# Performance work log

Measured on AMD Instinct MI355X. Metric: run time of the kernel, lower is better.

The kernel has to match this reference:

```python
import jax, jax.numpy as jnp
import numpy as np

B, S, H = 2, 1024, 4096
NH, DH, NKV = 32, 128, 2          # heads, head_dim, kv groups
ROT = DH // 2                      # 64: GLM rotates first half of head dim
GROUP = NH // NKV                  # 16 query heads per kv group
SCALE = DH ** -0.5


def glm_rope(x, pos):
    """GLM interleaved rotary on first ROT dims. x: [B,S,h,DH], pos: [B,S] int."""
    rot, rest = x[..., :ROT], x[..., ROT:]
    inv_freq = 1.0 / (10000.0 ** (jnp.arange(0, ROT, 2, dtype=jnp.float32) / ROT))  # [ROT/2]
    ang = pos.astype(jnp.float32)[:, :, None] * inv_freq[None, None, :]             # [B,S,ROT/2]
    cos = jnp.cos(ang)[:, :, None, :]
    sin = jnp.sin(ang)[:, :, None, :]
    x0, x1 = rot[..., 0::2], rot[..., 1::2]
    o0 = x0 * cos - x1 * sin
    o1 = x1 * cos + x0 * sin
    rot_out = jnp.stack([o0, o1], axis=-1).reshape(rot.shape)
    return jnp.concatenate([rot_out, rest], axis=-1)


def setup_inputs() -> dict:
    key = jax.random.key(0)
    k1, k2, k3, k4 = jax.random.split(key, 4)
    return {
        "hidden_states": jax.random.normal(k1, (B, S, H), jnp.float32) * 0.02,
        "position_ids": jnp.arange(B * S, dtype=jnp.int32).reshape(B, S) % S,
        "W_qkv": jax.random.normal(k2, (H, NH * DH + 2 * NKV * DH), jnp.float32) * 0.02,
        "b_qkv": jax.random.normal(k3, (NH * DH + 2 * NKV * DH,), jnp.float32) * 0.02,
        "W_dense": jax.random.normal(k4, (NH * DH, H), jnp.float32) * 0.02,
    }


def reference(hidden_states, position_ids, W_qkv, b_qkv, W_dense):
    qkv = hidden_states @ W_qkv + b_qkv                              # [B,S,4608]
    q = qkv[..., : NH * DH].reshape(B, S, NH, DH)
    k = qkv[..., NH * DH : NH * DH + NKV * DH].reshape(B, S, NKV, DH)
    v = qkv[..., NH * DH + NKV * DH :].reshape(B, S, NKV, DH)

    q = glm_rope(q, position_ids)
    k = glm_rope(k, position_ids)

    # GQA: expand kv groups to all heads
    k = jnp.repeat(k, GROUP, axis=2)                                 # [B,S,NH,DH]
    v = jnp.repeat(v, GROUP, axis=2)

    scores = jnp.einsum("bqhd,bkhd->bhqk", q, k) * SCALE             # [B,NH,S,S]
    causal = jnp.tril(jnp.ones((S, S), dtype=bool))
    scores = jnp.where(causal[None, None], scores, jnp.finfo(scores.dtype).min)
    probs = jax.nn.softmax(scores, axis=-1)
    ctx = jnp.einsum("bhqk,bkhd->bqhd", probs, v).reshape(B, S, NH * DH)
    return ctx @ W_dense                                             # [B,S,H]
```

## Files before the change

kernel.cpp:

```cpp
#include <hip/hip_runtime.h>

#define B_    2
#define S_    1024
#define H_    4096
#define NH_   32
#define DH_   128
#define NKV_  2
#define GROUP_ 16
#define ROT_  64
#define NQKV_ 4608
#define SCALE_ 0.08838834764831845f
#define KVB   64

typedef __attribute__((ext_vector_type(8))) short bf16x8;
typedef __attribute__((ext_vector_type(4))) float f32x4;

typedef __attribute__((address_space(1))) const void* gptr_t;
typedef __attribute__((address_space(3))) void* lptr_t;

__device__ __forceinline__ unsigned short f2bf(float f) {
    unsigned int u = __builtin_bit_cast(unsigned int, f);
    u += 0x7FFFu + ((u >> 16) & 1u);
    return (unsigned short)(u >> 16);
}
__device__ __forceinline__ unsigned int pack2bf(float a, float b) {
    return (unsigned int)f2bf(a) | ((unsigned int)f2bf(b) << 16);
}

__global__ void k_f32_to_bf16(const float* __restrict__ in,
                              unsigned short* __restrict__ out, int n4) {
    int i = blockIdx.x * blockDim.x + threadIdx.x;
    if (i >= n4) return;
    const float4 v = reinterpret_cast<const float4*>(in)[i];
    ushort4 o;
    o.x = f2bf(v.x); o.y = f2bf(v.y); o.z = f2bf(v.z); o.w = f2bf(v.w);
    reinterpret_cast<ushort4*>(out)[i] = o;
}

__global__ __launch_bounds__(256) void k_transpose_bf16(
    const float* __restrict__ in, unsigned short* __restrict__ out,
    int K, int N) {
    __shared__ float tile[64][69];
    const int n0 = blockIdx.x * 64, k0 = blockIdx.y * 64;
    const int t = threadIdx.x;
    const int lk = t >> 4, ln4 = (t & 15) * 4;
    #pragma unroll
    for (int i = 0; i < 4; i++) {
        const float4 v = *reinterpret_cast<const float4*>(
            in + (size_t)(k0 + lk + i * 16) * N + n0 + ln4);
        tile[lk + i * 16][ln4 + 0] = v.x;
        tile[lk + i * 16][ln4 + 1] = v.y;
        tile[lk + i * 16][ln4 + 2] = v.z;
        tile[lk + i * 16][ln4 + 3] = v.w;
    }
    __syncthreads();
    const int n = t >> 2, kc = (t & 3) * 16;
    unsigned short tmp[16];
    #pragma unroll
    for (int j = 0; j < 16; j++) tmp[j] = f2bf(tile[kc + j][n]);
    unsigned short* dst = out + (size_t)(n0 + n) * K + k0 + kc;
    *reinterpret_cast<uint4*>(dst)     = *reinterpret_cast<uint4*>(tmp);
    *reinterpret_cast<uint4*>(dst + 8) = *reinterpret_cast<uint4*>(tmp + 8);
}

__global__ void k_rope_tab(const int* __restrict__ pos_ids,
                           float2* __restrict__ tab) {
    const int idx = blockIdx.x * blockDim.x + threadIdx.x;
    if (idx >= B_ * S_ * 32) return;
    const int t = idx >> 5, pr = idx & 31;
    const float freq = exp2f(-0.41524101186092f * (float)pr);
    float sn, cs;
    sincosf((float)pos_ids[t] * freq, &sn, &cs);
    tab[idx] = make_float2(cs, sn);
}

template<int MODE>
__global__ __launch_bounds__(256, 2) void k_gemm(
    const unsigned short* __restrict__ A,
    const unsigned short* __restrict__ Bt,
    const float* __restrict__ bias,
    float* __restrict__ Cf,
    const float2* __restrict__ ctab,
    unsigned short* __restrict__ Qh,
    unsigned short* __restrict__ Kh,
    unsigned short* __restrict__ Vt,
    int M, int N, int K)
{
    __shared__ __align__(16) char lds[2][32768];

    const int tid  = threadIdx.x;
    const int wave = tid >> 6, lane = tid & 63;
    const int lrow = lane & 15, lhi = lane >> 4;
    const int wm = (wave >> 1) * 64, wn = (wave & 1) * 64;
    const size_t a_row0 = (size_t)blockIdx.y * 128;
    const size_t b_col0 = (size_t)blockIdx.x * 128;

    const size_t strideK = (size_t)K * 2;
    const char* Asrc = (const char*)A + (a_row0 + (tid >> 3)) * strideK;
    const char* Bsrc = (const char*)Bt + (b_col0 + (tid >> 3)) * strideK;
    const int swz_src = ((tid & 7) * 16) ^ (((tid >> 3) & 7) << 4);
    const int dst_off = tid * 16;

    f32x4 acc[4][4] = {};
    const int nt = K >> 6;

    #pragma unroll
    for (int j = 0; j < 4; j++) {
        __builtin_amdgcn_global_load_lds(
            (gptr_t)(Asrc + (size_t)j * 32 * strideK + swz_src),
            (lptr_t)(lds[0] + j * 4096 + dst_off), 16, 0, 0);
        __builtin_amdgcn_global_load_lds(
            (gptr_t)(Bsrc + (size_t)j * 32 * strideK + swz_src),
            (lptr_t)(lds[0] + 16384 + j * 4096 + dst_off), 16, 0, 0);
    }

    int cur = 0;
    for (int t = 0; t < nt; t++) {
        if (t + 1 < nt) {
            const size_t kb = (size_t)(t + 1) * 128;
            #pragma unroll
            for (int j = 0; j < 4; j++) {
                __builtin_amdgcn_global_load_lds(
                    (gptr_t)(Asrc + (size_t)j * 32 * strideK + kb + swz_src),
                    (lptr_t)(lds[cur ^ 1] + j * 4096 + dst_off), 16, 0, 0);
                __builtin_amdgcn_global_load_lds(
                    (gptr_t)(Bsrc + (size_t)j * 32 * strideK + kb + swz_src),
                    (lptr_t)(lds[cur ^ 1] + 16384 + j * 4096 + dst_off), 16, 0, 0);
            }
            asm volatile("s_waitcnt vmcnt(8)" ::: "memory");
        } else {
            asm volatile("s_waitcnt vmcnt(0)" ::: "memory");
        }
        __builtin_amdgcn_s_barrier();

        const char* La = lds[cur];
        const char* Lb = lds[cur] + 16384;
        bf16x8 af[4][2], bfr[4][2];
        #pragma unroll
        for (int i = 0; i < 4; i++) {
            const int fr = wm + i * 16 + lrow;
            af[i][0] = *(const bf16x8*)(La + fr * 128 + ((lhi * 16) ^ ((fr & 7) << 4)));
            af[i][1] = *(const bf16x8*)(La + fr * 128 + ((64 + lhi * 16) ^ ((fr & 7) << 4)));
        }
        #pragma unroll
        for (int j = 0; j < 4; j++) {
            const int br = wn + j * 16 + lrow;
            bfr[j][0] = *(const bf16x8*)(Lb + br * 128 + ((lhi * 16) ^ ((br & 7) << 4)));
            bfr[j][1] = *(const bf16x8*)(Lb + br * 128 + ((64 + lhi * 16) ^ ((br & 7) << 4)));
        }
        #pragma unroll
        for (int i = 0; i < 4; i++)
            #pragma unroll
            for (int j = 0; j < 4; j++) {
                acc[i][j] = __builtin_amdgcn_mfma_f32_16x16x32_bf16(
                    af[i][0], bfr[j][0], acc[i][j], 0, 0, 0);
                acc[i][j] = __builtin_amdgcn_mfma_f32_16x16x32_bf16(
                    af[i][1], bfr[j][1], acc[i][j], 0, 0, 0);
            }
        __builtin_amdgcn_s_barrier();
        cur ^= 1;
    }

    if (MODE == 0) {
        #pragma unroll
        for (int i = 0; i < 4; i++)
            #pragma unroll
            for (int j = 0; j < 4; j++) {
                const size_t grow0 = a_row0 + wm + i * 16 + lhi * 4;
                const size_t gcol  = b_col0 + wn + j * 16 + lrow;
                const float bi = bias ? bias[gcol] : 0.f;
                #pragma unroll
                for (int r = 0; r < 4; r++)
                    Cf[(grow0 + r) * N + gcol] = acc[i][j][r] + bi;
            }
    } else {
        const int bx = (int)blockIdx.x;
        const size_t bb = a_row0 >> 10;
        if (bx >= 34) {
            const int g = bx - 34;
            #pragma unroll
            for (int i = 0; i < 4; i++)
                #pragma unroll
                for (int j = 0; j < 4; j++) {
                    const int dloc = wn + j * 16 + lrow;
                    const float bi = bias[b_col0 + dloc];
                    const size_t row0 = a_row0 + wm + i * 16 + lhi * 4;
                    unsigned short* dst =
                        Vt + ((bb * NKV_ + g) * DH_ + dloc) * S_ + (row0 & 1023);
                    *reinterpret_cast<uint2*>(dst) = make_uint2(
                        pack2bf(acc[i][j][0] + bi, acc[i][j][1] + bi),
                        pack2bf(acc[i][j][2] + bi, acc[i][j][3] + bi));
                }
        } else {
            unsigned short* lds_c = (unsigned short*)&lds[0][0];
            #pragma unroll
            for (int i = 0; i < 4; i++)
                #pragma unroll
                for (int j = 0; j < 4; j++) {
                    const int dloc = wn + j * 16 + lrow;
                    const float bi = bias[b_col0 + dloc];
                    const int rloc0 = wm + i * 16 + lhi * 4;
                    float v[4];
                    #pragma unroll
                    for (int r = 0; r < 4; r++) v[r] = acc[i][j][r] + bi;
                    if (dloc < 64) {
                        const int pr = dloc >> 1;
                        #pragma unroll
                        for (int r = 0; r < 4; r++) {
                            const float2 cs = ctab[(a_row0 + rloc0 + r) * 32 + pr];
                            const float partner = __shfl_xor(v[r], 1);
                            v[r] = (dloc & 1) ? (v[r] * cs.x + partner * cs.y)
                                              : (v[r] * cs.x - partner * cs.y);
                        }
                    }
                    #pragma unroll
                    for (int r = 0; r < 4; r++)
                        lds_c[(rloc0 + r) * 128 + dloc] = f2bf(v[r]);
                }
            __syncthreads();
            unsigned short* base = (bx < 32)
                ? Qh + ((bb * NH_ + bx) * S_ + (a_row0 & 1023)) * DH_
                : Kh + ((bb * NKV_ + (bx - 32)) * S_ + (a_row0 & 1023)) * DH_;
            const int off = tid * 64;
            #pragma unroll
            for (int c = 0; c < 8; c++)
                *reinterpret_cast<uint4*>(base + off + c * 8) =
                    *reinterpret_cast<const uint4*>(lds_c + off + c * 8);
        }
    }
}

__global__ __launch_bounds__(256) void k_attn(
    const unsigned short* __restrict__ Qh,
    const unsigned short* __restrict__ Kh,
    const unsigned short* __restrict__ Vt,
    unsigned short* __restrict__ ctx)
{
    __shared__ __align__(16) char lds_kt[2][16384];
    __shared__ __align__(16) char lds_vt[16384];
    __shared__ __align__(16) char lds_p[4][2048];

    const int tid  = threadIdx.x;
    const int wave = tid >> 6, lane = tid & 63;
    const int lrow = lane & 15, lhi = lane >> 4;
    char* myp = lds_p[wave];

    const int blk  = blockIdx.x;
    const int pair = blk & 7;
    const int h    = (blk >> 3) & 31;
    const int b    = blk >> 8;
    const int g    = h >> 4;

    const char* Kbase = (const char*)(Kh + (size_t)((b * NKV_ + g) * S_) * DH_);
    const char* Vbase = (const char*)(Vt + (size_t)((b * NKV_ + g) * DH_) * S_);

    const int kcol = lrow * 16;
    const int vrow_l = lane >> 3;
    const int vcol = (lane & 7) * 16;

    for (int half = 0; half < 2; half++) {
        const int qt = half ? (15 - pair) : pair;
        const int q0 = qt * 64 + wave * 16;
        const int ntiles = qt + 1;
        const int q_glob = q0 + lrow;

        #pragma unroll
        for (int i = 0; i < 4; i++) {
            const int ci = wave * 4 + i;
            const int r  = ci * 4 + lhi;
            __builtin_amdgcn_global_load_lds(
                (gptr_t)(Kbase + (size_t)r * 256 + (kcol ^ ((r & 7) << 4))),
                (lptr_t)(lds_kt[0] + ci * 1024), 16, 0, 0);
        }
        const unsigned short* Qp = Qh + ((size_t)((b * NH_ + h) * S_) + q0) * DH_;
        bf16x8 a_q[4];
        #pragma unroll
        for (int ks = 0; ks < 4; ks++)
            a_q[ks] = *(const bf16x8*)(Qp + (size_t)lrow * DH_ + ks * 32 + lhi * 8);
        asm volatile("s_waitcnt vmcnt(0)" ::: "memory");
        __builtin_amdgcn_s_barrier();

        float m_run = -1e30f, l_run = 0.f;
        f32x4 o_acc[8] = {};
        int cur = 0;

        for (int t = 0; t < ntiles; t++) {
            const bool has_next = (t + 1 < ntiles);
            #pragma unroll
            for (int i = 0; i < 4; i++) {
                const int ci = wave * 4 + i;
                const int r  = ci * 8 + vrow_l;
                __builtin_amdgcn_global_load_lds(
                    (gptr_t)(Vbase + (size_t)r * (S_ * 2) + t * (KVB * 2)
                             + (vcol ^ ((r & 7) << 4))),
                    (lptr_t)(lds_vt + ci * 1024), 16, 0, 0);
            }
            if (has_next) {
                const char* ksrc = Kbase + (size_t)(t + 1) * 16384;
                #pragma unroll
                for (int i = 0; i < 4; i++) {
                    const int ci = wave * 4 + i;
                    const int r  = ci * 4 + lhi;
                    __builtin_amdgcn_global_load_lds(
                        (gptr_t)(ksrc + (size_t)r * 256 + (kcol ^ ((r & 7) << 4))),
                        (lptr_t)(lds_kt[cur ^ 1] + ci * 1024), 16, 0, 0);
                }
            }
            f32x4 s_acc[4] = {};
            #pragma unroll
            for (int sub = 0; sub < 4; sub++) {
                const int r = sub * 16 + lrow;
                #pragma unroll
                for (int ks = 0; ks < 4; ks++) {
                    const bf16x8 a_k = *(const bf16x8*)(
                        lds_kt[cur] + r * 256 + ((ks * 64 + lhi * 16) ^ ((r & 7) << 4)));
                    s_acc[sub] = __builtin_amdgcn_mfma_f32_16x16x32_bf16(
                        a_k, a_q[ks], s_acc[sub], 0, 0, 0);
                }
            }
            float pv[16];
            float mx = -1e30f;
            if (!has_next) {
                #pragma unroll
                for (int sub = 0; sub < 4; sub++)
                    #pragma unroll
                    for (int r = 0; r < 4; r++) {
                        const int kvg = t * KVB + sub * 16 + lhi * 4 + r;
                        float sv = s_acc[sub][r] * SCALE_;
                        if (kvg > q_glob) sv = -1e30f;
                        pv[sub * 4 + r] = sv;
                        mx = fmaxf(mx, sv);
                    }
            } else {
                #pragma unroll
                for (int sub = 0; sub < 4; sub++)
                    #pragma unroll
                    for (int r = 0; r < 4; r++) {
                        const float sv = s_acc[sub][r] * SCALE_;
                        pv[sub * 4 + r] = sv;
                        mx = fmaxf(mx, sv);
                    }
            }
            mx = fmaxf(mx, __shfl_xor(mx, 16));
            mx = fmaxf(mx, __shfl_xor(mx, 32));
            const float mnew = fmaxf(m_run, mx);
            const float scale = __expf(m_run - mnew);
            m_run = mnew;
            float sm = 0.f;
            #pragma unroll
            for (int i = 0; i < 16; i++) {
                const float e = __expf(pv[i] - mnew);
                pv[i] = e;
                sm += e;
            }
            sm += __shfl_xor(sm, 16);
            sm += __shfl_xor(sm, 32);
            l_run = l_run * scale + sm;
            #pragma unroll
            for (int d = 0; d < 8; d++) {
                o_acc[d][0] *= scale; o_acc[d][1] *= scale;
                o_acc[d][2] *= scale; o_acc[d][3] *= scale;
            }
            #pragma unroll
            for (int sub = 0; sub < 4; sub++) {
                const int off = (lrow * 128 + sub * 32 + lhi * 8) ^ ((lrow & 7) << 4);
                *reinterpret_cast<uint2*>(myp + off) = make_uint2(
                    pack2bf(pv[sub * 4 + 0], pv[sub * 4 + 1]),
                    pack2bf(pv[sub * 4 + 2], pv[sub * 4 + 3]));
            }
            bf16x8 a_p[2];
            #pragma unroll
            for (int frag = 0; frag < 2; frag++) {
                const int off = (lrow * 128 + frag * 64 + lhi * 16) ^ ((lrow & 7) << 4);
                a_p[frag] = *reinterpret_cast<const bf16x8*>(myp + off);
            }
            if (has_next) asm volatile("s_waitcnt vmcnt(4)" ::: "memory");
            else          asm volatile("s_waitcnt vmcnt(0)" ::: "memory");
            __builtin_amdgcn_s_barrier();
            #pragma unroll
            for (int d = 0; d < 8; d++) {
                const int r = d * 16 + lrow;
                #pragma unroll
                for (int frag = 0; frag < 2; frag++) {
                    const bf16x8 a_v = *(const bf16x8*)(
                        lds_vt + r * 128 + ((frag * 64 + lhi * 16) ^ ((r & 7) << 4)));
                    o_acc[d] = __builtin_amdgcn_mfma_f32_16x16x32_bf16(
                        a_v, a_p[frag], o_acc[d], 0, 0, 0);
                }
            }
            asm volatile("s_waitcnt vmcnt(0)" ::: "memory");
            __builtin_amdgcn_s_barrier();
            cur ^= 1;
        }
        const float inv = 1.f / l_run;
        const size_t row = (size_t)b * S_ + q0 + lrow;
        #pragma unroll
        for (int d = 0; d < 8; d++) {
            unsigned short* dst = ctx + row * (NH_ * DH_) + h * DH_ + d * 16 + lhi * 4;
            *reinterpret_cast<uint2*>(dst) = make_uint2(
                pack2bf(o_acc[d][0] * inv, o_acc[d][1] * inv),
                pack2bf(o_acc[d][2] * inv, o_acc[d][3] * inv));
        }
    }
}

extern "C" void kernel_launch(void* const* d_in, const int* in_sizes, int n_in,
                              void* d_out, int out_size, void* d_ws, size_t ws_size,
                              hipStream_t stream)
{
    const float* hidden  = (const float*)d_in[0];
    const int*   pos_ids = (const int*)d_in[1];
    const float* W_qkv   = (const float*)d_in[2];
    const float* b_qkv   = (const float*)d_in[3];
    const float* W_dense = (const float*)d_in[4];
    float* out = (float*)d_out;

    char* ws = (char*)d_ws;
    unsigned short* Xbf = (unsigned short*)(ws);
    unsigned short* Wqt = (unsigned short*)(ws + 16777216);
    unsigned short* Wdt = (unsigned short*)(ws + 54525952);
    float2*         ctab= (float2*)        (ws + 88080384);
    unsigned short* Qh  = (unsigned short*)(ws + 125829120);
    unsigned short* Kh  = (unsigned short*)(ws + 142606336);
    unsigned short* Vt  = (unsigned short*)(ws + 143654912);
    unsigned short* Ctx = (unsigned short*)(ws + 144703488);

    const int M = B_ * S_;

    k_f32_to_bf16<<<(M * H_ / 4 + 255) / 256, 256, 0, stream>>>(hidden, Xbf, M * H_ / 4);
    k_rope_tab<<<(M * 32 + 255) / 256, 256, 0, stream>>>(pos_ids, ctab);
    k_transpose_bf16<<<dim3(NQKV_ / 64, H_ / 64), 256, 0, stream>>>(W_qkv, Wqt, H_, NQKV_);
    k_transpose_bf16<<<dim3(H_ / 64, H_ / 64), 256, 0, stream>>>(W_dense, Wdt, H_, H_);
    k_gemm<1><<<dim3(NQKV_ / 128, M / 128), 256, 0, stream>>>(
        Xbf, Wqt, b_qkv, nullptr, ctab, Qh, Kh, Vt, M, NQKV_, H_);
    k_attn<<<B_ * NH_ * 8, 256, 0, stream>>>(Qh, Kh, Vt, Ctx);
    k_gemm<0><<<dim3(H_ / 128, M / 128), 256, 0, stream>>>(
        Ctx, Wdt, nullptr, out, nullptr, nullptr, nullptr, nullptr, M, H_, H_);
}
```

Baseline: 269.8 us.

## Use four-stage K=32 LDS ring with one barrier per step in GEMM

Rebuilds the GEMM mainloop from a double-buffered K=64 tile with two barriers per iteration into a 4-slot ring of K=32 tiles, prefetched three stages ahead with graded vmcnt waits and a single barrier per step. The LDS layout packs two rows per 128-byte line with a new XOR swizzle. The aim is deeper latency hiding of global loads and fewer barriers. In exchange it doubles the number of iterations and adds a sync before the epilogue reuses LDS.

```diff
diff --git a/kernel.cpp b/kernel.cpp
--- a/kernel.cpp
+++ b/kernel.cpp
@@ -86,7 +86,7 @@
     unsigned short* __restrict__ Vt,
     int M, int N, int K)
 {
-    __shared__ __align__(16) char lds[2][32768];
+    __shared__ __align__(16) char lds[4 * 16384];
 
     const int tid  = threadIdx.x;
     const int wave = tid >> 6, lane = tid & 63;
@@ -96,70 +96,66 @@
     const size_t b_col0 = (size_t)blockIdx.x * 128;
 
     const size_t strideK = (size_t)K * 2;
-    const char* Asrc = (const char*)A + (a_row0 + (tid >> 3)) * strideK;
-    const char* Bsrc = (const char*)Bt + (b_col0 + (tid >> 3)) * strideK;
-    const int swz_src = ((tid & 7) * 16) ^ (((tid >> 3) & 7) << 4);
-    const int dst_off = tid * 16;
+    const char* Abase = (const char*)A + a_row0 * strideK;
+    const char* Bbase = (const char*)Bt + b_col0 * strideK;
+
+    const int q0 = tid, q1 = tid + 256;
+    const int v0_ = q0 >> 3, cl0 = ((q0 & 7) * 16) ^ ((v0_ & 7) << 4);
+    const int v1_ = q1 >> 3, cl1 = ((q1 & 7) * 16) ^ ((v1_ & 7) << 4);
+    const size_t aoff0 = (size_t)(v0_ * 2 + (cl0 >> 6)) * strideK + (cl0 & 63);
+    const size_t aoff1 = (size_t)(v1_ * 2 + (cl1 >> 6)) * strideK + (cl1 & 63);
 
     f32x4 acc[4][4] = {};
-    const int nt = K >> 6;
-
-    #pragma unroll
-    for (int j = 0; j < 4; j++) {
-        __builtin_amdgcn_global_load_lds(
-            (gptr_t)(Asrc + (size_t)j * 32 * strideK + swz_src),
-            (lptr_t)(lds[0] + j * 4096 + dst_off), 16, 0, 0);
-        __builtin_amdgcn_global_load_lds(
-            (gptr_t)(Bsrc + (size_t)j * 32 * strideK + swz_src),
-            (lptr_t)(lds[0] + 16384 + j * 4096 + dst_off), 16, 0, 0);
+    const int nt = K >> 5;
+
+#define STAGE_(tt) { \
+    const size_t kk = (size_t)(tt) * 64; \
+    char* sl = lds + ((tt) & 3) * 16384; \
+    __builtin_amdgcn_global_load_lds((gptr_t)(Abase + aoff0 + kk), \
+        (lptr_t)(sl + tid * 16), 16, 0, 0); \
+    __builtin_amdgcn_global_load_lds((gptr_t)(Abase + aoff1 + kk), \
+        (lptr_t)(sl + 4096 + tid * 16), 16, 0, 0); \
+    __builtin_amdgcn_global_load_lds((gptr_t)(Bbase + aoff0 + kk), \
+        (lptr_t)(sl + 8192 + tid * 16), 16, 0, 0); \
+    __builtin_amdgcn_global_load_lds((gptr_t)(Bbase + aoff1 + kk), \
+        (lptr_t)(sl + 12288 + tid * 16), 16, 0, 0); }
+
+    STAGE_(0);
+    if (1 < nt) STAGE_(1);
+    if (2 < nt) STAGE_(2);
+
+    for (int t = 0; t < nt; t++) {
+        if (t + 2 < nt)      asm volatile("s_waitcnt vmcnt(8)" ::: "memory");
+        else if (t + 1 < nt) asm volatile("s_waitcnt vmcnt(4)" ::: "memory");
+        else                 asm volatile("s_waitcnt vmcnt(0)" ::: "memory");
+        __builtin_amdgcn_s_barrier();
+        if (t + 3 < nt) STAGE_(t + 3);
+
+        const char* sA = lds + (t & 3) * 16384;
+        const char* sB = sA + 8192;
+        bf16x8 af[4], bfr[4];
+        #pragma unroll
+        for (int mi = 0; mi < 4; mi++) {
+            const int r = wm + mi * 16 + lrow;
+            const int v = r >> 1;
+            const int cl = ((r & 1) << 6) + (lhi << 4);
+            af[mi] = *(const bf16x8*)(sA + v * 128 + (cl ^ ((v & 7) << 4)));
+        }
+        #pragma unroll
+        for (int nj = 0; nj < 4; nj++) {
+            const int r = wn + nj * 16 + lrow;
+            const int v = r >> 1;
+            const int cl = ((r & 1) << 6) + (lhi << 4);
+            bfr[nj] = *(const bf16x8*)(sB + v * 128 + (cl ^ ((v & 7) << 4)));
+        }
+        #pragma unroll
+        for (int mi = 0; mi < 4; mi++)
+            #pragma unroll
+            for (int nj = 0; nj < 4; nj++)
+                acc[mi][nj] = __builtin_amdgcn_mfma_f32_16x16x32_bf16(
+                    af[mi], bfr[nj], acc[mi][nj], 0, 0, 0);
     }
-
-    int cur = 0;
-    for (int t = 0; t < nt; t++) {
-        if (t + 1 < nt) {
-            const size_t kb = (size_t)(t + 1) * 128;
-            #pragma unroll
-            for (int j = 0; j < 4; j++) {
-                __builtin_amdgcn_global_load_lds(
-                    (gptr_t)(Asrc + (size_t)j * 32 * strideK + kb + swz_src),
-                    (lptr_t)(lds[cur ^ 1] + j * 4096 + dst_off), 16, 0, 0);
-                __builtin_amdgcn_global_load_lds(
-                    (gptr_t)(Bsrc + (size_t)j * 32 * strideK + kb + swz_src),
-                    (lptr_t)(lds[cur ^ 1] + 16384 + j * 4096 + dst_off), 16, 0, 0);
-            }
-            asm volatile("s_waitcnt vmcnt(8)" ::: "memory");
-        } else {
-            asm volatile("s_waitcnt vmcnt(0)" ::: "memory");
-        }
-        __builtin_amdgcn_s_barrier();
-
-        const char* La = lds[cur];
-        const char* Lb = lds[cur] + 16384;
-        bf16x8 af[4][2], bfr[4][2];
-        #pragma unroll
-        for (int i = 0; i < 4; i++) {
-            const int fr = wm + i * 16 + lrow;
-            af[i][0] = *(const bf16x8*)(La + fr * 128 + ((lhi * 16) ^ ((fr & 7) << 4)));
-            af[i][1] = *(const bf16x8*)(La + fr * 128 + ((64 + lhi * 16) ^ ((fr & 7) << 4)));
-        }
-        #pragma unroll
-        for (int j = 0; j < 4; j++) {
-            const int br = wn + j * 16 + lrow;
-            bfr[j][0] = *(const bf16x8*)(Lb + br * 128 + ((lhi * 16) ^ ((br & 7) << 4)));
-            bfr[j][1] = *(const bf16x8*)(Lb + br * 128 + ((64 + lhi * 16) ^ ((br & 7) << 4)));
-        }
-        #pragma unroll
-        for (int i = 0; i < 4; i++)
-            #pragma unroll
-            for (int j = 0; j < 4; j++) {
-                acc[i][j] = __builtin_amdgcn_mfma_f32_16x16x32_bf16(
-                    af[i][0], bfr[j][0], acc[i][j], 0, 0, 0);
-                acc[i][j] = __builtin_amdgcn_mfma_f32_16x16x32_bf16(
-                    af[i][1], bfr[j][1], acc[i][j], 0, 0, 0);
-            }
-        __builtin_amdgcn_s_barrier();
-        cur ^= 1;
-    }
+#undef STAGE_
 
     if (MODE == 0) {
         #pragma unroll
@@ -192,7 +188,8 @@
                         pack2bf(acc[i][j][2] + bi, acc[i][j][3] + bi));
                 }
         } else {
-            unsigned short* lds_c = (unsigned short*)&lds[0][0];
+            __syncthreads();
+            unsigned short* lds_c = (unsigned short*)&lds[0];
             #pragma unroll
             for (int i = 0; i < 4; i++)
                 #pragma unroll
```

New measurement: 298.1 us. 10.5% more time.
